# Optimization experiments

Hardware: AMD Instinct MI355X
Metric: run time of the kernel (lower is better)

## Reference

```python
import jax, jax.numpy as jnp
import numpy as np

# FPMA (Mitchell-style) approximate bf16 multiply: a*b is approximated by
# integer-adding the exponent+mantissa bit fields of the two bf16 operands
# and subtracting the exponent bias offset (0x3F80 for bf16). Sign is XOR of
# sign bits. Underflow is flushed to zero; overflow clamped to max finite.
SIGN_MASK = 0x8000
MAG_MASK = 0x7FFF
BIAS_OFF = 0x3F80  # 127 << 7 (bf16 exponent bias in bit position)
MAX_FINITE = 0x7F7F
CHUNK = 4  # rows of the input processed per scan step (bounds the [C,N,K] intermediate)


def _fpma_matmul(x, w):
    """x: [M,K] bf16, w: [N,K] bf16 -> [M,N] fp32 accumulated approximate products."""
    xb = jax.lax.bitcast_convert_type(x, jnp.uint16).astype(jnp.int32)  # [M,K]
    wb = jax.lax.bitcast_convert_type(w, jnp.uint16).astype(jnp.int32)  # [N,K]
    M, K = xb.shape
    xs, xm = xb & SIGN_MASK, xb & MAG_MASK
    ws, wm = wb & SIGN_MASK, wb & MAG_MASK

    def block(args):
        bs, bm = args  # each [CHUNK, K]
        sign = bs[:, None, :] ^ ws[None]                      # [C,N,K]
        mag = bm[:, None, :] + wm[None] - BIAS_OFF            # approx exp+mant add
        mag = jnp.clip(mag, 0, MAX_FINITE)                    # flush underflow, clamp overflow
        is_zero = (bm[:, None, :] == 0) | (wm[None] == 0)     # exact-zero operands
        bits = jnp.where(is_zero, 0, sign | mag).astype(jnp.uint16)
        prod = jax.lax.bitcast_convert_type(bits, jnp.bfloat16)
        return prod.astype(jnp.float32).sum(-1)               # [C,N] fp32 accumulate

    xs_c = xs.reshape(M // CHUNK, CHUNK, K)
    xm_c = xm.reshape(M // CHUNK, CHUNK, K)
    out = jax.lax.map(block, (xs_c, xm_c))                    # [M//C, C, N]
    return out.reshape(M, -1)


def setup_inputs() -> dict:
    key = jax.random.key(0)
    k1, k2, k3 = jax.random.split(key, 3)
    M, K, N = 4096, 2048, 2048
    input = jax.random.normal(k1, (M, K), dtype=jnp.bfloat16)
    weight = (jax.random.normal(k2, (N, K), dtype=jnp.float32) * 0.02).astype(jnp.bfloat16)
    bias = (jax.random.normal(k3, (1, N), dtype=jnp.float32) * 0.02).astype(jnp.bfloat16)
    return {"input": input, "weight": weight, "bias": bias}


def reference(input, weight, bias):
    orig_shape = input.shape[:-1]
    x = input.reshape(-1, input.shape[-1])
    acc = _fpma_matmul(x, weight)                 # [M,N] fp32
    out = acc.astype(jnp.bfloat16) + bias         # bias added in bf16, as in the kernel wrapper
    return out.reshape(*orig_shape, weight.shape[0])
```

## Files before the change

### kernel.cpp

```cpp
#include <hip/hip_runtime.h>
#include <stdint.h>

typedef unsigned short v2u   __attribute__((ext_vector_type(2)));
typedef unsigned short u16x8 __attribute__((ext_vector_type(8)));
typedef short          s16x8 __attribute__((ext_vector_type(8)));
typedef float          f32x4 __attribute__((ext_vector_type(4)));

#define TM 64
#define TN 64

__device__ __forceinline__ uint32_t rnd_bf16(float f) {
    uint32_t u = __builtin_bit_cast(uint32_t, f);
    return (u + 0x7FFFu + ((u >> 16) & 1u)) >> 16;
}
__device__ __forceinline__ float bf16_to_f32(uint32_t bits16) {
    return __builtin_bit_cast(float, bits16 << 16);
}

__device__ __forceinline__ uint32_t pack_x(uint32_t w0, uint32_t w1) {
    uint32_t u = (w0 >> 16) | (w1 & 0xFFFF0000u);
    const v2u vfloor = {0x2000, 0x2000};
    v2u m = __builtin_bit_cast(v2u, u & 0x7FFF7FFFu);
    m = __builtin_elementwise_max(m, vfloor);
    uint32_t c = (u & 0x80008000u) ^ 0xC080C080u;
    v2u xp = m + __builtin_bit_cast(v2u, c);
    return __builtin_bit_cast(uint32_t, xp);
}
__device__ __forceinline__ uint32_t pack_w(uint32_t w0, uint32_t w1) {
    uint32_t v = (w0 >> 16) | (w1 & 0xFFFF0000u);
    const v2u vfloor = {0x2000, 0x2000};
    v2u m = __builtin_bit_cast(v2u, v & 0x7FFF7FFFu);
    m = __builtin_elementwise_max(m, vfloor);
    return __builtin_bit_cast(uint32_t, m) | (v & 0x80008000u);
}

__global__ void pack_kernel(const uint32_t* __restrict__ in,
                            uint32_t* __restrict__ out, int n4, int mode)
{
    int i = blockIdx.x * blockDim.x + threadIdx.x;
    const int stride = gridDim.x * blockDim.x;
    for (; i < n4; i += stride) {
        uint4 v = ((const uint4*)in)[i];
        uint2 o;
        if (mode == 0) { o.x = pack_x(v.x, v.y); o.y = pack_x(v.z, v.w); }
        else           { o.x = pack_w(v.x, v.y); o.y = pack_w(v.z, v.w); }
        ((uint2*)out)[i] = o;
    }
}

__global__ __launch_bounds__(256, 3)
void fpma_gemm_pre(const uint32_t* __restrict__ Xq,
                   const uint32_t* __restrict__ Wq,
                   const float*    __restrict__ Bias,
                   float* __restrict__ Out,
                   int M, int N, int K)
{
    __shared__ uint32_t Xp[2][2][64 * 16];
    __shared__ uint32_t Wp[2][2][64 * 16];

    const int tid  = threadIdx.x;
    const int lane = tid & 63;
    const int warp = tid >> 6;
    const int wm = warp >> 1, wn = warp & 1;
    const int m0 = blockIdx.y * TM;
    const int n0 = blockIdx.x * TN;

    const int cc = lane & 15;
    const int q  = lane >> 4;
    const int mi = cc >> 2;
    const int ni = cc & 3;

    const int xrd = (32 * wm + mi) * 16 + ((q ^ mi) << 2);
    int wrd[4];
    #pragma unroll
    for (int t = 0; t < 4; ++t)
        wrd[t] = (32 * wn + ni) * 16 + ((q ^ ni) << 2) + (((q + t) & 3) << 6);

    u16x8 bt[4];
    #pragma unroll
    for (int t = 0; t < 4; ++t) {
        unsigned short v = ((cc >> 2) == ((q + t) & 3)) ? (unsigned short)0x3F80
                                                        : (unsigned short)0;
        bt[t] = (u16x8){v, v, v, v, v, v, v, v};
    }

    const int srow = tid >> 2;
    const int soct = tid & 3;
    const int Kp = K >> 1;
    const int swz = (soct ^ (srow & 3)) << 2;
    const uint32_t* xsrc = Xq + (size_t)(m0 + srow) * Kp + swz;
    const uint32_t* wsrc = Wq + (size_t)(n0 + srow) * Kp + swz;

    f32x4 acc[8][2];
    #pragma unroll
    for (int a = 0; a < 8; ++a)
        #pragma unroll
        for (int bg = 0; bg < 2; ++bg) acc[a][bg] = (f32x4){0.f, 0.f, 0.f, 0.f};

    __builtin_amdgcn_global_load_lds(xsrc,      &Xp[0][0][tid << 2], 16, 0, 0);
    __builtin_amdgcn_global_load_lds(xsrc + 16, &Xp[0][1][tid << 2], 16, 0, 0);
    __builtin_amdgcn_global_load_lds(wsrc,      &Wp[0][0][tid << 2], 16, 0, 0);
    __builtin_amdgcn_global_load_lds(wsrc + 16, &Wp[0][1][tid << 2], 16, 0, 0);
    xsrc += 32; wsrc += 32;
    __syncthreads();

    const int ksteps = K / 64;
    #pragma unroll 1
    for (int kt = 0; kt < ksteps; ++kt) {
        const int cur = kt & 1;
        if (kt + 1 < ksteps) {
            __builtin_amdgcn_global_load_lds(xsrc,      &Xp[cur ^ 1][0][tid << 2], 16, 0, 0);
            __builtin_amdgcn_global_load_lds(xsrc + 16, &Xp[cur ^ 1][1][tid << 2], 16, 0, 0);
            __builtin_amdgcn_global_load_lds(wsrc,      &Wp[cur ^ 1][0][tid << 2], 16, 0, 0);
            __builtin_amdgcn_global_load_lds(wsrc + 16, &Wp[cur ^ 1][1][tid << 2], 16, 0, 0);
            xsrc += 32; wsrc += 32;
        }

        __builtin_amdgcn_s_setprio(1);
        #pragma unroll
        for (int ks = 0; ks < 2; ++ks) {
            u16x8 xf[8];
            #pragma unroll
            for (int a = 0; a < 8; ++a)
                xf[a] = __builtin_bit_cast(u16x8,
                            *(const uint4*)&Xp[cur][ks][xrd + a * 64]);
            #pragma unroll
            for (int bg = 0; bg < 2; ++bg) {
                u16x8 wf[4];
                #pragma unroll
                for (int t = 0; t < 4; ++t)
                    wf[t] = __builtin_bit_cast(u16x8,
                                *(const uint4*)&Wp[cur][ks][wrd[t] + bg * 256]);
                #pragma unroll
                for (int t = 0; t < 4; ++t)
                    #pragma unroll
                    for (int a = 0; a < 8; ++a) {
                        u16x8 p = xf[a] + wf[t];
                        acc[a][bg] = __builtin_amdgcn_mfma_f32_16x16x32_bf16(
                            __builtin_bit_cast(s16x8, p),
                            __builtin_bit_cast(s16x8, bt[t]),
                            acc[a][bg], 0, 0, 0);
                    }
            }
        }
        __builtin_amdgcn_s_setprio(0);
        __syncthreads();
    }

    const int g = cc >> 2;
    f32x4 bias_[2];
    #pragma unroll
    for (int bg = 0; bg < 2; ++bg)
        bias_[bg] = *(const f32x4*)&Bias[n0 + 32 * wn + 16 * bg + 4 * g];

    #pragma unroll
    for (int a = 0; a < 8; ++a) {
        if ((cc & 3) == (a & 3)) {
            #pragma unroll
            for (int bg = 0; bg < 2; ++bg) {
                float o[4];
                #pragma unroll
                for (int j = 0; j < 4; ++j)
                    o[j] = bf16_to_f32(rnd_bf16(
                               bf16_to_f32(rnd_bf16(acc[a][bg][j])) + bias_[bg][j]));
                const size_t row = (size_t)(m0 + 32 * wm + 4 * a + q) * N;
                *(float4*)&Out[row + n0 + 32 * wn + 16 * bg + 4 * g] =
                    make_float4(o[0], o[1], o[2], o[3]);
            }
        }
    }
}

__global__ __launch_bounds__(256, 3)
void fpma_gemm_fb(const uint32_t* __restrict__ X, const uint32_t* __restrict__ Wt,
                  const float* __restrict__ Bias, float* __restrict__ Out,
                  int M, int N, int K)
{
    __shared__ uint32_t Xp[2][64 * 16];
    __shared__ uint32_t Wp[2][64 * 16];

    const int tid  = threadIdx.x;
    const int lane = tid & 63;
    const int warp = tid >> 6;
    const int wm = warp >> 1, wn = warp & 1;
    const int m0 = blockIdx.y * TM;
    const int n0 = blockIdx.x * TN;
    const int cc = lane & 15;
    const int q  = lane >> 4;
    const int mi = cc >> 2;
    const int ni = cc & 3;
    const int xrd = (32 * wm + mi) * 16 + ((q ^ mi) << 2);
    int wrd[4];
    #pragma unroll
    for (int t = 0; t < 4; ++t)
        wrd[t] = (32 * wn + ni) * 16 + ((q ^ ni) << 2) + (((q + t) & 3) << 6);
    u16x8 bt[4];
    #pragma unroll
    for (int t = 0; t < 4; ++t) {
        unsigned short v = ((cc >> 2) == ((q + t) & 3)) ? (unsigned short)0x3F80
                                                        : (unsigned short)0;
        bt[t] = (u16x8){v, v, v, v, v, v, v, v};
    }
    const int srow = tid >> 2;
    const int soct = tid & 3;
    const uint32_t* xptr = X  + (size_t)(m0 + srow) * K + soct * 8;
    const uint32_t* wptr = Wt + (size_t)(n0 + srow) * K + soct * 8;
    const int st = srow * 16 + ((soct ^ (srow & 3)) << 2);

    f32x4 acc[8][2];
    #pragma unroll
    for (int a = 0; a < 8; ++a)
        #pragma unroll
        for (int bg = 0; bg < 2; ++bg) acc[a][bg] = (f32x4){0.f, 0.f, 0.f, 0.f};

    {
        uint4 a0 = *(const uint4*)(xptr), a1 = *(const uint4*)(xptr + 4);
        uint4 b0 = *(const uint4*)(wptr), b1 = *(const uint4*)(wptr + 4);
        *(uint4*)&Xp[0][st] = (uint4){pack_x(a0.x,a0.y), pack_x(a0.z,a0.w),
                                      pack_x(a1.x,a1.y), pack_x(a1.z,a1.w)};
        *(uint4*)&Wp[0][st] = (uint4){pack_w(b0.x,b0.y), pack_w(b0.z,b0.w),
                                      pack_w(b1.x,b1.y), pack_w(b1.z,b1.w)};
    }
    uint4 gx0 = {0,0,0,0}, gx1 = {0,0,0,0}, gw0 = {0,0,0,0}, gw1 = {0,0,0,0};
    const int ksteps = K / 32;
    if (ksteps > 1) {
        xptr += 32; wptr += 32;
        gx0 = *(const uint4*)(xptr); gx1 = *(const uint4*)(xptr + 4);
        gw0 = *(const uint4*)(wptr); gw1 = *(const uint4*)(wptr + 4);
    }
    __syncthreads();

    #pragma unroll 1
    for (int kt = 0; kt < ksteps; ++kt) {
        const int cur = kt & 1;
        if (kt + 1 < ksteps) {
            *(uint4*)&Xp[cur ^ 1][st] = (uint4){pack_x(gx0.x,gx0.y), pack_x(gx0.z,gx0.w),
                                                pack_x(gx1.x,gx1.y), pack_x(gx1.z,gx1.w)};
            *(uint4*)&Wp[cur ^ 1][st] = (uint4){pack_w(gw0.x,gw0.y), pack_w(gw0.z,gw0.w),
                                                pack_w(gw1.x,gw1.y), pack_w(gw1.z,gw1.w)};
            if (kt + 2 < ksteps) {
                xptr += 32; wptr += 32;
                gx0 = *(const uint4*)(xptr); gx1 = *(const uint4*)(xptr + 4);
                gw0 = *(const uint4*)(wptr); gw1 = *(const uint4*)(wptr + 4);
            }
        }
        u16x8 xf[8];
        #pragma unroll
        for (int a = 0; a < 8; ++a)
            xf[a] = __builtin_bit_cast(u16x8, *(const uint4*)&Xp[cur][xrd + a * 64]);
        #pragma unroll
        for (int bg = 0; bg < 2; ++bg) {
            u16x8 wf[4];
            #pragma unroll
            for (int t = 0; t < 4; ++t)
                wf[t] = __builtin_bit_cast(u16x8, *(const uint4*)&Wp[cur][wrd[t] + bg * 256]);
            #pragma unroll
            for (int t = 0; t < 4; ++t)
                #pragma unroll
                for (int a = 0; a < 8; ++a) {
                    u16x8 p = xf[a] + wf[t];
                    acc[a][bg] = __builtin_amdgcn_mfma_f32_16x16x32_bf16(
                        __builtin_bit_cast(s16x8, p),
                        __builtin_bit_cast(s16x8, bt[t]), acc[a][bg], 0, 0, 0);
                }
        }
        __syncthreads();
    }

    const int g = cc >> 2;
    f32x4 bias_[2];
    #pragma unroll
    for (int bg = 0; bg < 2; ++bg)
        bias_[bg] = *(const f32x4*)&Bias[n0 + 32 * wn + 16 * bg + 4 * g];
    #pragma unroll
    for (int a = 0; a < 8; ++a) {
        if ((cc & 3) == (a & 3)) {
            #pragma unroll
            for (int bg = 0; bg < 2; ++bg) {
                float o[4];
                #pragma unroll
                for (int j = 0; j < 4; ++j)
                    o[j] = bf16_to_f32(rnd_bf16(
                               bf16_to_f32(rnd_bf16(acc[a][bg][j])) + bias_[bg][j]));
                const size_t row = (size_t)(m0 + 32 * wm + 4 * a + q) * N;
                *(float4*)&Out[row + n0 + 32 * wn + 16 * bg + 4 * g] =
                    make_float4(o[0], o[1], o[2], o[3]);
            }
        }
    }
}

extern "C" void kernel_launch(void* const* d_in, const int* in_sizes, int n_in,
                              void* d_out, int out_size, void* d_ws, size_t ws_size,
                              hipStream_t stream) {
    (void)n_in; (void)out_size;
    const uint32_t* X = (const uint32_t*)d_in[0];
    const uint32_t* W = (const uint32_t*)d_in[1];
    const float*    B = (const float*)d_in[2];
    float* O = (float*)d_out;

    int N = in_sizes[2];
    int K = (N > 0) ? in_sizes[1] / N : 0;
    int M = (K > 0) ? in_sizes[0] / K : 0;
    if (N <= 0 || K <= 0 || M <= 0 ||
        (long long)N * K != (long long)in_sizes[1] ||
        (long long)M * K != (long long)in_sizes[0] ||
        (M % TM) || (N % TN) || (K % 64)) {
        M = 4096; K = 2048; N = 2048;
    }

    const size_t xq_words = (size_t)M * (K / 2);
    const size_t wq_words = (size_t)N * (K / 2);
    const size_t need = (xq_words + wq_words) * 4;

    dim3 grid(N / TN, M / TM);
    if (d_ws != nullptr && ws_size >= need) {
        uint32_t* Xq = (uint32_t*)d_ws;
        uint32_t* Wq = Xq + xq_words;
        pack_kernel<<<1024, 256, 0, stream>>>(X, Xq, (int)(xq_words / 2), 0);
        pack_kernel<<<1024, 256, 0, stream>>>(W, Wq, (int)(wq_words / 2), 1);
        fpma_gemm_pre<<<grid, 256, 0, stream>>>(Xq, Wq, B, O, M, N, K);
    } else {
        fpma_gemm_fb<<<grid, 256, 0, stream>>>(X, W, B, O, M, N, K);
    }
}
```

Measured before the change: 506.5 us.

## Offload one of four MFMA reduction groups to VALU dot2 instructions

One of the four selector-matrix MFMA passes is replaced by v_dot2_f32_bf16 reductions on the vector ALU into per-lane scalar partial sums. Those partials are redistributed through LDS at the end and added to the MFMA accumulators before rounding. The aim is to balance work between the matrix core and the VALU so the MFMA pipe is no longer the sole bottleneck. The cost is extra VALU instructions and registers, an LDS exchange in the epilogue, and possible changes in the order of floating-point summation.

```diff
diff --git a/kernel.cpp b/kernel.cpp
--- a/kernel.cpp
+++ b/kernel.cpp
@@ -76,13 +76,14 @@
     for (int t = 0; t < 4; ++t)
         wrd[t] = (32 * wn + ni) * 16 + ((q ^ ni) << 2) + (((q + t) & 3) << 6);
 
-    u16x8 bt[4];
-    #pragma unroll
-    for (int t = 0; t < 4; ++t) {
+    u16x8 bt[3];
+    #pragma unroll
+    for (int t = 0; t < 3; ++t) {
         unsigned short v = ((cc >> 2) == ((q + t) & 3)) ? (unsigned short)0x3F80
                                                         : (unsigned short)0;
         bt[t] = (u16x8){v, v, v, v, v, v, v, v};
     }
+    const float ones_pair = __builtin_bit_cast(float, 0x3F803F80u);
 
     const int srow = tid >> 2;
     const int soct = tid & 3;
@@ -92,10 +93,14 @@
     const uint32_t* wsrc = Wq + (size_t)(n0 + srow) * Kp + swz;
 
     f32x4 acc[8][2];
+    float S[8][2];
     #pragma unroll
     for (int a = 0; a < 8; ++a)
         #pragma unroll
-        for (int bg = 0; bg < 2; ++bg) acc[a][bg] = (f32x4){0.f, 0.f, 0.f, 0.f};
+        for (int bg = 0; bg < 2; ++bg) {
+            acc[a][bg] = (f32x4){0.f, 0.f, 0.f, 0.f};
+            S[a][bg] = 0.f;
+        }
 
     __builtin_amdgcn_global_load_lds(xsrc,      &Xp[0][0][tid << 2], 16, 0, 0);
     __builtin_amdgcn_global_load_lds(xsrc + 16, &Xp[0][1][tid << 2], 16, 0, 0);
@@ -132,7 +137,7 @@
                     wf[t] = __builtin_bit_cast(u16x8,
                                 *(const uint4*)&Wp[cur][ks][wrd[t] + bg * 256]);
                 #pragma unroll
-                for (int t = 0; t < 4; ++t)
+                for (int t = 0; t < 3; ++t)
                     #pragma unroll
                     for (int a = 0; a < 8; ++a) {
                         u16x8 p = xf[a] + wf[t];
@@ -141,13 +146,45 @@
                             __builtin_bit_cast(s16x8, bt[t]),
                             acc[a][bg], 0, 0, 0);
                     }
+                #pragma unroll
+                for (int a = 0; a < 8; ++a) {
+                    u16x8 p = xf[a] + wf[3];
+                    uint4 pb = __builtin_bit_cast(uint4, p);
+                    asm("v_dot2_f32_bf16 %0, %1, %2, %0" : "+v"(S[a][bg])
+                        : "v"(__builtin_bit_cast(float, pb.x)), "v"(ones_pair));
+                    asm("v_dot2_f32_bf16 %0, %1, %2, %0" : "+v"(S[a][bg])
+                        : "v"(__builtin_bit_cast(float, pb.y)), "v"(ones_pair));
+                    asm("v_dot2_f32_bf16 %0, %1, %2, %0" : "+v"(S[a][bg])
+                        : "v"(__builtin_bit_cast(float, pb.z)), "v"(ones_pair));
+                    asm("v_dot2_f32_bf16 %0, %1, %2, %0" : "+v"(S[a][bg])
+                        : "v"(__builtin_bit_cast(float, pb.w)), "v"(ones_pair));
+                }
             }
         }
         __builtin_amdgcn_s_setprio(0);
         __syncthreads();
     }
 
+    __syncthreads();
+    uint32_t* sb = &Xp[0][0][0] + (warp << 10);
+    #pragma unroll
+    for (int a = 0; a < 8; ++a)
+        #pragma unroll
+        for (int bg = 0; bg < 2; ++bg)
+            sb[lane * 16 + a * 2 + bg] = __builtin_bit_cast(uint32_t, S[a][bg]);
+
     const int g = cc >> 2;
+    const int ls = (((g + 1) & 3) << 4) + (q << 2);
+    float Sp[2][2][4];
+    #pragma unroll
+    for (int ah = 0; ah < 2; ++ah)
+        #pragma unroll
+        for (int bg = 0; bg < 2; ++bg)
+            #pragma unroll
+            for (int j = 0; j < 4; ++j)
+                Sp[ah][bg][j] = __builtin_bit_cast(float,
+                    sb[(ls + j) * 16 + ((cc & 3) + 4 * ah) * 2 + bg]);
+
     f32x4 bias_[2];
     #pragma unroll
     for (int bg = 0; bg < 2; ++bg)
@@ -160,9 +197,11 @@
             for (int bg = 0; bg < 2; ++bg) {
                 float o[4];
                 #pragma unroll
-                for (int j = 0; j < 4; ++j)
+                for (int j = 0; j < 4; ++j) {
+                    float tot = acc[a][bg][j] + Sp[a >> 2][bg][j];
                     o[j] = bf16_to_f32(rnd_bf16(
-                               bf16_to_f32(rnd_bf16(acc[a][bg][j])) + bias_[bg][j]));
+                               bf16_to_f32(rnd_bf16(tot)) + bias_[bg][j]));
+                }
                 const size_t row = (size_t)(m0 + 32 * wm + 4 * a + q) * N;
                 *(float4*)&Out[row + n0 + 32 * wn + 16 * bg + 4 * g] =
                     make_float4(o[0], o[1], o[2], o[3]);
```

New measurement: 539.6 us. 1.07x slower.
